# Kernel optimization log

Measured on AMD Instinct MI355X. Metric: run time of the kernel, lower is better.

Reference implementation:

```python
import jax, jax.numpy as jnp
import numpy as np

B, S, D, H = 8, 1024, 1024, 16
DEPTH = D // H  # 64


def setup_inputs() -> dict:
    key = jax.random.key(0)
    ks = jax.random.split(key, 12)
    s = 1.0 / np.sqrt(D)
    return {
        "Q": jax.random.normal(ks[0], (B, S, D), jnp.float32),
        "K": jax.random.normal(ks[1], (B, S, D), jnp.float32),
        "V": jax.random.normal(ks[2], (B, S, D), jnp.float32),
        "mask": jnp.zeros((B, 1, 1, S), jnp.float32),
        "Wq": jax.random.normal(ks[3], (D, D), jnp.float32) * s,
        "bq": jnp.zeros((D,), jnp.float32),
        "Wk": jax.random.normal(ks[4], (D, D), jnp.float32) * s,
        "bk": jnp.zeros((D,), jnp.float32),
        "Wv": jax.random.normal(ks[5], (D, D), jnp.float32) * s,
        "bv": jnp.zeros((D,), jnp.float32),
        "Wo": jax.random.normal(ks[6], (D, D), jnp.float32) * s,
        "bo": jnp.zeros((D,), jnp.float32),
    }


def _split_heads(x):
    # [B,S,D] -> [B,H,S,depth]
    b, s, _ = x.shape
    return x.reshape(b, s, H, DEPTH).transpose(0, 2, 1, 3)


def reference(Q, K, V, mask, Wq, bq, Wk, bk, Wv, bv, Wo, bo):
    q = _split_heads(Q @ Wq + bq)  # [B,H,S,depth]
    k = _split_heads(K @ Wk + bk)
    v = _split_heads(V @ Wv + bv)
    scale = 1.0 / jnp.sqrt(jnp.asarray(DEPTH, q.dtype))
    scores = jnp.einsum('bhqd,bhkd->bhqk', q, k) * scale  # [B,H,Sq,Sk]
    scores = scores + mask * (-1e9)
    attn = jax.nn.softmax(scores, axis=-1)
    out = jnp.einsum('bhqk,bhkd->bhqd', attn, v)  # [B,H,S,depth]
    out = out.transpose(0, 2, 1, 3).reshape(Q.shape[0], Q.shape[1], D)
    out = out @ Wo + bo
    return out, attn
```

## Files before the change

### kernel.cpp

```cpp
#include <hip/hip_runtime.h>

#define Bb 8
#define Ss 1024
#define Dd 1024
#define Hh 16
#define DEPTHh 64
#define BSD (Bb*Ss*Dd)
#define DDn (Dd*Dd)

typedef __bf16 bf16x8 __attribute__((ext_vector_type(8)));
typedef float  f32x4  __attribute__((ext_vector_type(4)));

__device__ __forceinline__ unsigned short f2bf(float f){
  unsigned u = __float_as_uint(f);
  u = (u + 0x7fffu + ((u >> 16) & 1u)) >> 16;
  return (unsigned short)u;
}
__device__ __forceinline__ float bf2f(unsigned short h){
  return __uint_as_float(((unsigned)h) << 16);
}

__global__ __launch_bounds__(256) void cvt_bf16(const float4* __restrict__ in,
                                                ushort4* __restrict__ out, int n4){
  int i = blockIdx.x*256 + threadIdx.x;
  if (i >= n4) return;
  float4 v = in[i];
  ushort4 o; o.x = f2bf(v.x); o.y = f2bf(v.y); o.z = f2bf(v.z); o.w = f2bf(v.w);
  out[i] = o;
}

__global__ __launch_bounds__(256) void transpose_w(const float* __restrict__ W,
                                                   ushort* __restrict__ WT){
  __shared__ float tl[32][33];
  int tx = threadIdx.x, ty = threadIdx.y;
  int bx = blockIdx.x*32, by = blockIdx.y*32;
  #pragma unroll
  for (int i=0;i<32;i+=8) tl[ty+i][tx] = W[(by+ty+i)*Dd + bx+tx];
  __syncthreads();
  #pragma unroll
  for (int i=0;i<32;i+=8) WT[(bx+ty+i)*Dd + by+tx] = f2bf(tl[tx][ty+i]);
}

__global__ __launch_bounds__(512) void transpose_v(const ushort* __restrict__ vh,
                                                   ushort* __restrict__ vt){
  __shared__ ushort tl[64][65];
  int tx = threadIdx.x, ty = threadIdx.y;
  long base = (long)blockIdx.y * 65536;
  int s0 = blockIdx.x*64;
  #pragma unroll
  for (int i=0;i<64;i+=8) tl[ty+i][tx] = vh[base + (long)(s0+ty+i)*64 + tx];
  __syncthreads();
  #pragma unroll
  for (int i=0;i<64;i+=8) vt[base + (long)(ty+i)*1024 + s0 + tx] = tl[tx][ty+i];
}

enum { M_PROJ=0, M_FINAL=3 };

template<int MODE>
__global__ __launch_bounds__(256) void gemm_bt(
    const ushort* __restrict__ Aall, const ushort* __restrict__ Ball,
    int lda, int ldb, int K, long sA, long sB,
    float* __restrict__ outf, ushort* __restrict__ outh,
    const float* __restrict__ aux)
{
  __shared__ ushort As[64][40];
  __shared__ ushort Bs[64][40];
  const int z = blockIdx.z;
  const ushort* A  = Aall + (long)z*sA;
  const ushort* Bp = Ball + (long)z*sB;
  const int m0 = blockIdx.x*64, n0 = blockIdx.y*64;
  const int t = threadIdx.x;
  const int lane = t & 63, wave = t >> 6;
  const int wm = (wave>>1)*32, wn = (wave&1)*32;
  const int q = lane>>4, l16 = lane&15;
  const int srow = t>>2, scol = (t&3)*8;

  f32x4 acc[2][2] = {};

  for (int k0=0; k0<K; k0+=32){
    uint4 av = *(const uint4*)(A  + (long)(m0+srow)*lda + k0 + scol);
    uint4 bv = *(const uint4*)(Bp + (long)(n0+srow)*ldb + k0 + scol);
    __syncthreads();
    *(uint4*)(&As[srow][scol]) = av;
    *(uint4*)(&Bs[srow][scol]) = bv;
    __syncthreads();
    bf16x8 a0 = *(const bf16x8*)(&As[wm      + l16][q*8]);
    bf16x8 a1 = *(const bf16x8*)(&As[wm + 16 + l16][q*8]);
    bf16x8 b0 = *(const bf16x8*)(&Bs[wn      + l16][q*8]);
    bf16x8 b1 = *(const bf16x8*)(&Bs[wn + 16 + l16][q*8]);
    acc[0][0] = __builtin_amdgcn_mfma_f32_16x16x32_bf16(a0,b0,acc[0][0],0,0,0);
    acc[0][1] = __builtin_amdgcn_mfma_f32_16x16x32_bf16(a0,b1,acc[0][1],0,0,0);
    acc[1][0] = __builtin_amdgcn_mfma_f32_16x16x32_bf16(a1,b0,acc[1][0],0,0,0);
    acc[1][1] = __builtin_amdgcn_mfma_f32_16x16x32_bf16(a1,b1,acc[1][1],0,0,0);
  }

  #pragma unroll
  for (int ti=0; ti<2; ti++)
  #pragma unroll
  for (int tj=0; tj<2; tj++)
  #pragma unroll
  for (int r=0; r<4; r++){
    float v = acc[ti][tj][r];
    const int row = m0 + wm + ti*16 + q*4 + r;
    const int col = n0 + wn + tj*16 + l16;
    if (MODE == M_PROJ){
      v += aux[col];
      const int b = row>>10, s = row&1023, h = col>>6, d = col&63;
      outh[((long)((b*Hh + h)*Ss + s)<<6) + d] = f2bf(v);
    } else {
      v += aux[col];
      outf[(long)row*Dd + col] = v;
    }
  }
}

__global__ __launch_bounds__(256) void attn_fused(
    const ushort* __restrict__ qh,
    const ushort* __restrict__ kh,
    const ushort* __restrict__ vt,
    const float*  __restrict__ mask,
    float* __restrict__ attn_f,
    ushort* __restrict__ concat)
{
  __shared__ __align__(16) ushort qs[64][72];
  __shared__ __align__(16) ushort ks[64][72];
  __shared__ __align__(16) ushort vs[64][72];
  __shared__ __align__(16) ushort ps[64][72];
  __shared__ float red_m[2][64];
  __shared__ float red_l[2][64];

  const int z = blockIdx.z;
  const int b = z >> 4, h = z & 15;
  const int t = threadIdx.x;
  const int lane = t & 63, wave = t >> 6;
  const int wm = (wave >> 1) * 32;
  const int wc = wave & 1;
  const int wn = wc * 32;
  const int q = lane >> 4, l16 = lane & 15;
  const int srow = t >> 2, sc = (t & 3) * 8;

  const ushort* qz = qh + ((long)z << 16);
  const ushort* kz = kh + ((long)z << 16);
  const ushort* vz = vt + ((long)z << 16);
  const int q0 = blockIdx.x * 64;

  {
    const ushort* src = qz + (long)(q0 + srow) * 64 + sc;
    *(uint4*)(&qs[srow][sc])      = *(const uint4*)(src);
    *(uint4*)(&qs[srow][sc + 32]) = *(const uint4*)(src + 32);
  }

  float m_ln[2][4], l_ln[2][4];
  #pragma unroll
  for (int ti=0; ti<2; ti++)
  #pragma unroll
  for (int r=0; r<4; r++){ m_ln[ti][r] = -1e30f; l_ln[ti][r] = 0.f; }

  for (int s = 0; s < 16; ++s){
    const int k0 = s * 64;
    const ushort* ksrc = kz + (long)(k0 + srow) * 64 + sc;
    uint4 kv0 = *(const uint4*)(ksrc);
    uint4 kv1 = *(const uint4*)(ksrc + 32);
    __syncthreads();
    *(uint4*)(&ks[srow][sc])      = kv0;
    *(uint4*)(&ks[srow][sc + 32]) = kv1;
    __syncthreads();

    f32x4 accs[2][2] = {};
    #pragma unroll
    for (int kk=0; kk<2; ++kk){
      bf16x8 a0 = *(const bf16x8*)(&qs[wm      + l16][kk*32 + q*8]);
      bf16x8 a1 = *(const bf16x8*)(&qs[wm + 16 + l16][kk*32 + q*8]);
      bf16x8 b0 = *(const bf16x8*)(&ks[wn      + l16][kk*32 + q*8]);
      bf16x8 b1 = *(const bf16x8*)(&ks[wn + 16 + l16][kk*32 + q*8]);
      accs[0][0] = __builtin_amdgcn_mfma_f32_16x16x32_bf16(a0,b0,accs[0][0],0,0,0);
      accs[0][1] = __builtin_amdgcn_mfma_f32_16x16x32_bf16(a0,b1,accs[0][1],0,0,0);
      accs[1][0] = __builtin_amdgcn_mfma_f32_16x16x32_bf16(a1,b0,accs[1][0],0,0,0);
      accs[1][1] = __builtin_amdgcn_mfma_f32_16x16x32_bf16(a1,b1,accs[1][1],0,0,0);
    }
    const float mk0 = mask[(b<<10) + k0 + wn + l16]      * (-1e9f);
    const float mk1 = mask[(b<<10) + k0 + wn + 16 + l16] * (-1e9f);
    #pragma unroll
    for (int ti=0; ti<2; ti++)
    #pragma unroll
    for (int r=0; r<4; r++){
      const float s0 = accs[ti][0][r]*0.125f + mk0;
      const float s1 = accs[ti][1][r]*0.125f + mk1;
      const float mn = fmaxf(m_ln[ti][r], fmaxf(s0, s1));
      l_ln[ti][r] = l_ln[ti][r]*__expf(m_ln[ti][r]-mn)
                  + __expf(s0-mn) + __expf(s1-mn);
      m_ln[ti][r] = mn;
    }
  }

  #pragma unroll
  for (int ti=0; ti<2; ti++)
  #pragma unroll
  for (int r=0; r<4; r++){
    float m = m_ln[ti][r], l = l_ln[ti][r];
    #pragma unroll
    for (int off=1; off<16; off<<=1){
      float om = __shfl_xor(m, off, 64);
      float ol = __shfl_xor(l, off, 64);
      float mn = fmaxf(m, om);
      l = l*__expf(m-mn) + ol*__expf(om-mn);
      m = mn;
    }
    m_ln[ti][r] = m; l_ln[ti][r] = l;
  }
  if (l16 == 0){
    #pragma unroll
    for (int ti=0; ti<2; ti++)
    #pragma unroll
    for (int r=0; r<4; r++){
      const int row = wm + ti*16 + q*4 + r;
      red_m[wc][row] = m_ln[ti][r];
      red_l[wc][row] = l_ln[ti][r];
    }
  }
  __syncthreads();
  float m_fin[2][4], li[2][4];
  #pragma unroll
  for (int ti=0; ti<2; ti++)
  #pragma unroll
  for (int r=0; r<4; r++){
    const int row = wm + ti*16 + q*4 + r;
    const float m0 = red_m[0][row], m1 = red_m[1][row];
    const float l0 = red_l[0][row], l1 = red_l[1][row];
    const float mt = fmaxf(m0, m1);
    const float lt = l0*__expf(m0-mt) + l1*__expf(m1-mt);
    m_fin[ti][r] = mt;
    li[ti][r] = 1.0f / lt;
  }

  f32x4 accp[2][2] = {};
  for (int s = 0; s < 16; ++s){
    const int k0 = s * 64;
    const ushort* ksrc = kz + (long)(k0 + srow) * 64 + sc;
    const ushort* vsrc = vz + (long)srow * 1024 + k0 + sc;
    uint4 kv0 = *(const uint4*)(ksrc);
    uint4 kv1 = *(const uint4*)(ksrc + 32);
    uint4 vv0 = *(const uint4*)(vsrc);
    uint4 vv1 = *(const uint4*)(vsrc + 32);
    __syncthreads();
    *(uint4*)(&ks[srow][sc])      = kv0;
    *(uint4*)(&ks[srow][sc + 32]) = kv1;
    *(uint4*)(&vs[srow][sc])      = vv0;
    *(uint4*)(&vs[srow][sc + 32]) = vv1;
    __syncthreads();

    f32x4 accs[2][2] = {};
    #pragma unroll
    for (int kk=0; kk<2; ++kk){
      bf16x8 a0 = *(const bf16x8*)(&qs[wm      + l16][kk*32 + q*8]);
      bf16x8 a1 = *(const bf16x8*)(&qs[wm + 16 + l16][kk*32 + q*8]);
      bf16x8 b0 = *(const bf16x8*)(&ks[wn      + l16][kk*32 + q*8]);
      bf16x8 b1 = *(const bf16x8*)(&ks[wn + 16 + l16][kk*32 + q*8]);
      accs[0][0] = __builtin_amdgcn_mfma_f32_16x16x32_bf16(a0,b0,accs[0][0],0,0,0);
      accs[0][1] = __builtin_amdgcn_mfma_f32_16x16x32_bf16(a0,b1,accs[0][1],0,0,0);
      accs[1][0] = __builtin_amdgcn_mfma_f32_16x16x32_bf16(a1,b0,accs[1][0],0,0,0);
      accs[1][1] = __builtin_amdgcn_mfma_f32_16x16x32_bf16(a1,b1,accs[1][1],0,0,0);
    }
    const float mk0 = mask[(b<<10) + k0 + wn + l16]      * (-1e9f);
    const float mk1 = mask[(b<<10) + k0 + wn + 16 + l16] * (-1e9f);
    #pragma unroll
    for (int ti=0; ti<2; ti++)
    #pragma unroll
    for (int r=0; r<4; r++){
      const int row = wm + ti*16 + q*4 + r;
      const float p0 = __expf(accs[ti][0][r]*0.125f + mk0 - m_fin[ti][r]) * li[ti][r];
      const float p1 = __expf(accs[ti][1][r]*0.125f + mk1 - m_fin[ti][r]) * li[ti][r];
      float* arow = attn_f + (((long)z<<20) + ((long)(q0+row)<<10) + k0);
      arow[wn + l16]      = p0;
      arow[wn + 16 + l16] = p1;
      ps[row][wn + l16]      = f2bf(p0);
      ps[row][wn + 16 + l16] = f2bf(p1);
    }
    __syncthreads();
    #pragma unroll
    for (int kk=0; kk<2; ++kk){
      bf16x8 a0 = *(const bf16x8*)(&ps[wm      + l16][kk*32 + q*8]);
      bf16x8 a1 = *(const bf16x8*)(&ps[wm + 16 + l16][kk*32 + q*8]);
      bf16x8 b0 = *(const bf16x8*)(&vs[wn      + l16][kk*32 + q*8]);
      bf16x8 b1 = *(const bf16x8*)(&vs[wn + 16 + l16][kk*32 + q*8]);
      accp[0][0] = __builtin_amdgcn_mfma_f32_16x16x32_bf16(a0,b0,accp[0][0],0,0,0);
      accp[0][1] = __builtin_amdgcn_mfma_f32_16x16x32_bf16(a0,b1,accp[0][1],0,0,0);
      accp[1][0] = __builtin_amdgcn_mfma_f32_16x16x32_bf16(a1,b0,accp[1][0],0,0,0);
      accp[1][1] = __builtin_amdgcn_mfma_f32_16x16x32_bf16(a1,b1,accp[1][1],0,0,0);
    }
  }

  #pragma unroll
  for (int mi=0; mi<2; mi++)
  #pragma unroll
  for (int nj=0; nj<2; nj++)
  #pragma unroll
  for (int r=0; r<4; r++){
    const int row = q0 + wm + mi*16 + q*4 + r;
    const int d   = wn + nj*16 + l16;
    concat[(((long)(b<<10) + row)<<10) + (h<<6) + d] = f2bf(accp[mi][nj][r]);
  }
}

extern "C" void kernel_launch(void* const* d_in, const int* in_sizes, int n_in,
                              void* d_out, int out_size, void* d_ws, size_t ws_size,
                              hipStream_t stream)
{
  (void)in_sizes; (void)n_in; (void)out_size; (void)ws_size;
  const float* Q    = (const float*)d_in[0];
  const float* Kin  = (const float*)d_in[1];
  const float* V    = (const float*)d_in[2];
  const float* mask = (const float*)d_in[3];
  const float* Wq   = (const float*)d_in[4];
  const float* bq   = (const float*)d_in[5];
  const float* Wk   = (const float*)d_in[6];
  const float* bk   = (const float*)d_in[7];
  const float* Wv   = (const float*)d_in[8];
  const float* bv   = (const float*)d_in[9];
  const float* Wo   = (const float*)d_in[10];
  const float* bo   = (const float*)d_in[11];
  float* out    = (float*)d_out;
  float* attn_f = out + (long)BSD;

  ushort* ws     = (ushort*)d_ws;
  ushort* Xq     = ws;
  ushort* Xk     = Xq  + (long)BSD;
  ushort* Xv     = Xk  + (long)BSD;
  ushort* WqT    = Xv  + (long)BSD;
  ushort* WkT    = WqT + (long)DDn;
  ushort* WvT    = WkT + (long)DDn;
  ushort* WoT    = WvT + (long)DDn;
  ushort* qh     = WoT + (long)DDn;
  ushort* kh     = qh  + (long)BSD;
  ushort* vt     = kh  + (long)BSD;
  ushort* vh     = vt  + (long)BSD;
  ushort* concat = Xq;

  cvt_bf16<<<dim3(BSD/4/256), 256, 0, stream>>>((const float4*)Q,   (ushort4*)Xq, BSD/4);
  cvt_bf16<<<dim3(BSD/4/256), 256, 0, stream>>>((const float4*)Kin, (ushort4*)Xk, BSD/4);
  cvt_bf16<<<dim3(BSD/4/256), 256, 0, stream>>>((const float4*)V,   (ushort4*)Xv, BSD/4);

  transpose_w<<<dim3(32,32), dim3(32,8), 0, stream>>>(Wq, WqT);
  transpose_w<<<dim3(32,32), dim3(32,8), 0, stream>>>(Wk, WkT);
  transpose_w<<<dim3(32,32), dim3(32,8), 0, stream>>>(Wv, WvT);
  transpose_w<<<dim3(32,32), dim3(32,8), 0, stream>>>(Wo, WoT);

  gemm_bt<M_PROJ><<<dim3(128,16,1), 256, 0, stream>>>(Xq, WqT, Dd, Dd, Dd, 0,0, nullptr, qh, bq);
  gemm_bt<M_PROJ><<<dim3(128,16,1), 256, 0, stream>>>(Xk, WkT, Dd, Dd, Dd, 0,0, nullptr, kh, bk);
  gemm_bt<M_PROJ><<<dim3(128,16,1), 256, 0, stream>>>(Xv, WvT, Dd, Dd, Dd, 0,0, nullptr, vh, bv);

  transpose_v<<<dim3(16,128), dim3(64,8), 0, stream>>>(vh, vt);

  attn_fused<<<dim3(16,1,128), 256, 0, stream>>>(qh, kh, vt, mask, attn_f, concat);

  gemm_bt<M_FINAL><<<dim3(128,16,1), 256, 0, stream>>>(concat, WoT, Dd, Dd, Dd,
                                                       0,0, out, nullptr, bo);
}
```

Baseline: 955.7 us.

## Use 128x128 GEMM tiles with direct-to-LDS loads and prefetch K/V in attention

Replaces the 64x64 projection GEMM with a 128x128 tile kernel that copies A/B straight into LDS via global_load_lds and keeps a 4x4 MFMA accumulator grid per wave. This raises data reuse per loaded tile and skips the register staging step. The attention kernel now computes K·Q^T with keys as rows, so per-query softmax statistics live in lanes and fewer shuffles are needed. It also switches to exp2 with folded scaling, caches the mask in LDS, register-prefetches the next K/V tile, and writes attention probabilities as float4. The larger GEMM accumulator raises register pressure, and the GEMM loop has no double buffering.

```diff
diff --git a/kernel.cpp b/kernel.cpp
--- a/kernel.cpp
+++ b/kernel.cpp
@@ -4,7 +4,6 @@
 #define Ss 1024
 #define Dd 1024
 #define Hh 16
-#define DEPTHh 64
 #define BSD (Bb*Ss*Dd)
 #define DDn (Dd*Dd)
 
@@ -16,8 +15,12 @@
   u = (u + 0x7fffu + ((u >> 16) & 1u)) >> 16;
   return (unsigned short)u;
 }
-__device__ __forceinline__ float bf2f(unsigned short h){
-  return __uint_as_float(((unsigned)h) << 16);
+__device__ __forceinline__ float fexp2(float x){ return __builtin_exp2f(x); }
+
+__device__ __forceinline__ void gload16(const ushort* g, ushort* l){
+  __builtin_amdgcn_global_load_lds(
+      (const __attribute__((address_space(1))) void*)g,
+      (__attribute__((address_space(3))) void*)l, 16, 0, 0);
 }
 
 __global__ __launch_bounds__(256) void cvt_bf16(const float4* __restrict__ in,
@@ -57,58 +60,64 @@
 enum { M_PROJ=0, M_FINAL=3 };
 
 template<int MODE>
-__global__ __launch_bounds__(256) void gemm_bt(
-    const ushort* __restrict__ Aall, const ushort* __restrict__ Ball,
-    int lda, int ldb, int K, long sA, long sB,
+__global__ __launch_bounds__(256) void gemm128(
+    const ushort* __restrict__ A, const ushort* __restrict__ B,
     float* __restrict__ outf, ushort* __restrict__ outh,
     const float* __restrict__ aux)
 {
-  __shared__ ushort As[64][40];
-  __shared__ ushort Bs[64][40];
-  const int z = blockIdx.z;
-  const ushort* A  = Aall + (long)z*sA;
-  const ushort* Bp = Ball + (long)z*sB;
-  const int m0 = blockIdx.x*64, n0 = blockIdx.y*64;
-  const int t = threadIdx.x;
-  const int lane = t & 63, wave = t >> 6;
-  const int wm = (wave>>1)*32, wn = (wave&1)*32;
+  __shared__ __align__(16) ushort As[128*32];
+  __shared__ __align__(16) ushort Bs[128*32];
+  const int t = threadIdx.x, lane = t & 63, wave = t >> 6;
+  const int m0 = blockIdx.x*128, n0 = blockIdx.y*128;
+  const int wm = (wave>>1)*64, wn = (wave&1)*64;
   const int q = lane>>4, l16 = lane&15;
-  const int srow = t>>2, scol = (t&3)*8;
-
-  f32x4 acc[2][2] = {};
-
-  for (int k0=0; k0<K; k0+=32){
-    uint4 av = *(const uint4*)(A  + (long)(m0+srow)*lda + k0 + scol);
-    uint4 bv = *(const uint4*)(Bp + (long)(n0+srow)*ldb + k0 + scol);
-    __syncthreads();
-    *(uint4*)(&As[srow][scol]) = av;
-    *(uint4*)(&Bs[srow][scol]) = bv;
-    __syncthreads();
-    bf16x8 a0 = *(const bf16x8*)(&As[wm      + l16][q*8]);
-    bf16x8 a1 = *(const bf16x8*)(&As[wm + 16 + l16][q*8]);
-    bf16x8 b0 = *(const bf16x8*)(&Bs[wn      + l16][q*8]);
-    bf16x8 b1 = *(const bf16x8*)(&Bs[wn + 16 + l16][q*8]);
-    acc[0][0] = __builtin_amdgcn_mfma_f32_16x16x32_bf16(a0,b0,acc[0][0],0,0,0);
-    acc[0][1] = __builtin_amdgcn_mfma_f32_16x16x32_bf16(a0,b1,acc[0][1],0,0,0);
-    acc[1][0] = __builtin_amdgcn_mfma_f32_16x16x32_bf16(a1,b0,acc[1][0],0,0,0);
-    acc[1][1] = __builtin_amdgcn_mfma_f32_16x16x32_bf16(a1,b1,acc[1][1],0,0,0);
-  }
-
-  #pragma unroll
-  for (int ti=0; ti<2; ti++)
-  #pragma unroll
-  for (int tj=0; tj<2; tj++)
-  #pragma unroll
-  for (int r=0; r<4; r++){
-    float v = acc[ti][tj][r];
-    const int row = m0 + wm + ti*16 + q*4 + r;
-    const int col = n0 + wn + tj*16 + l16;
+  const int row0 = t>>2, cc = (t&3)*8;
+
+  ushort* lA0 = As + wave*512;
+  ushort* lA1 = As + 2048 + wave*512;
+  ushort* lB0 = Bs + wave*512;
+  ushort* lB1 = Bs + 2048 + wave*512;
+  const ushort* gA0 = A + (long)(m0+row0)*Dd + cc;
+  const ushort* gA1 = A + (long)(m0+row0+64)*Dd + cc;
+  const ushort* gB0 = B + (long)(n0+row0)*Dd + cc;
+  const ushort* gB1 = B + (long)(n0+row0+64)*Dd + cc;
+
+  f32x4 acc[4][4] = {};
+
+  for (int k0=0; k0<Dd; k0+=32){
+    __syncthreads();
+    gload16(gA0+k0, lA0);
+    gload16(gA1+k0, lA1);
+    gload16(gB0+k0, lB0);
+    gload16(gB1+k0, lB1);
+    __syncthreads();
+    bf16x8 af[4], bfr[4];
+    #pragma unroll
+    for (int i=0;i<4;i++){
+      af[i]  = *(const bf16x8*)(As + (wm+i*16+l16)*32 + q*8);
+      bfr[i] = *(const bf16x8*)(Bs + (wn+i*16+l16)*32 + q*8);
+    }
+    #pragma unroll
+    for (int mi=0;mi<4;mi++)
+    #pragma unroll
+    for (int nj=0;nj<4;nj++)
+      acc[mi][nj] = __builtin_amdgcn_mfma_f32_16x16x32_bf16(af[mi],bfr[nj],acc[mi][nj],0,0,0);
+  }
+
+  #pragma unroll
+  for (int mi=0;mi<4;mi++)
+  #pragma unroll
+  for (int nj=0;nj<4;nj++)
+  #pragma unroll
+  for (int r=0;r<4;r++){
+    float v = acc[mi][nj][r];
+    const int row = m0 + wm + mi*16 + q*4 + r;
+    const int col = n0 + wn + nj*16 + l16;
+    v += aux[col];
     if (MODE == M_PROJ){
-      v += aux[col];
       const int b = row>>10, s = row&1023, h = col>>6, d = col&63;
       outh[((long)((b*Hh + h)*Ss + s)<<6) + d] = f2bf(v);
     } else {
-      v += aux[col];
       outf[(long)row*Dd + col] = v;
     }
   }
@@ -126,6 +135,7 @@
   __shared__ __align__(16) ushort ks[64][72];
   __shared__ __align__(16) ushort vs[64][72];
   __shared__ __align__(16) ushort ps[64][72];
+  __shared__ float msk[64];
   __shared__ float red_m[2][64];
   __shared__ float red_l[2][64];
 
@@ -143,6 +153,9 @@
   const ushort* kz = kh + ((long)z << 16);
   const ushort* vz = vt + ((long)z << 16);
   const int q0 = blockIdx.x * 64;
+  const float LOG2E = 1.44269504f;
+  const float SC2   = 0.125f * LOG2E;
+  const float MSC2  = -1e9f * LOG2E;
 
   {
     const ushort* src = qz + (long)(q0 + srow) * 64 + sc;
@@ -150,131 +163,147 @@
     *(uint4*)(&qs[srow][sc + 32]) = *(const uint4*)(src + 32);
   }
 
-  float m_ln[2][4], l_ln[2][4];
-  #pragma unroll
-  for (int ti=0; ti<2; ti++)
-  #pragma unroll
-  for (int r=0; r<4; r++){ m_ln[ti][r] = -1e30f; l_ln[ti][r] = 0.f; }
-
+  float m2[2], lsum[2];
+  m2[0] = m2[1] = -1e30f; lsum[0] = lsum[1] = 0.f;
+
+  uint4 kv0, kv1; float mv;
+  {
+    const ushort* ksrc = kz + (long)srow * 64 + sc;
+    kv0 = *(const uint4*)(ksrc); kv1 = *(const uint4*)(ksrc + 32);
+    mv = (t < 64) ? mask[(b<<10) + t] * MSC2 : 0.f;
+  }
   for (int s = 0; s < 16; ++s){
-    const int k0 = s * 64;
-    const ushort* ksrc = kz + (long)(k0 + srow) * 64 + sc;
-    uint4 kv0 = *(const uint4*)(ksrc);
-    uint4 kv1 = *(const uint4*)(ksrc + 32);
     __syncthreads();
     *(uint4*)(&ks[srow][sc])      = kv0;
     *(uint4*)(&ks[srow][sc + 32]) = kv1;
-    __syncthreads();
+    if (t < 64) msk[t] = mv;
+    __syncthreads();
+    if (s < 15){
+      const ushort* ksrc = kz + (long)((s+1)*64 + srow) * 64 + sc;
+      kv0 = *(const uint4*)(ksrc); kv1 = *(const uint4*)(ksrc + 32);
+      if (t < 64) mv = mask[(b<<10) + (s+1)*64 + t] * MSC2;
+    }
 
     f32x4 accs[2][2] = {};
     #pragma unroll
     for (int kk=0; kk<2; ++kk){
-      bf16x8 a0 = *(const bf16x8*)(&qs[wm      + l16][kk*32 + q*8]);
-      bf16x8 a1 = *(const bf16x8*)(&qs[wm + 16 + l16][kk*32 + q*8]);
-      bf16x8 b0 = *(const bf16x8*)(&ks[wn      + l16][kk*32 + q*8]);
-      bf16x8 b1 = *(const bf16x8*)(&ks[wn + 16 + l16][kk*32 + q*8]);
+      bf16x8 a0 = *(const bf16x8*)(&ks[wm      + l16][kk*32 + q*8]);
+      bf16x8 a1 = *(const bf16x8*)(&ks[wm + 16 + l16][kk*32 + q*8]);
+      bf16x8 b0 = *(const bf16x8*)(&qs[wn      + l16][kk*32 + q*8]);
+      bf16x8 b1 = *(const bf16x8*)(&qs[wn + 16 + l16][kk*32 + q*8]);
       accs[0][0] = __builtin_amdgcn_mfma_f32_16x16x32_bf16(a0,b0,accs[0][0],0,0,0);
       accs[0][1] = __builtin_amdgcn_mfma_f32_16x16x32_bf16(a0,b1,accs[0][1],0,0,0);
       accs[1][0] = __builtin_amdgcn_mfma_f32_16x16x32_bf16(a1,b0,accs[1][0],0,0,0);
       accs[1][1] = __builtin_amdgcn_mfma_f32_16x16x32_bf16(a1,b1,accs[1][1],0,0,0);
     }
-    const float mk0 = mask[(b<<10) + k0 + wn + l16]      * (-1e9f);
-    const float mk1 = mask[(b<<10) + k0 + wn + 16 + l16] * (-1e9f);
-    #pragma unroll
-    for (int ti=0; ti<2; ti++)
-    #pragma unroll
-    for (int r=0; r<4; r++){
-      const float s0 = accs[ti][0][r]*0.125f + mk0;
-      const float s1 = accs[ti][1][r]*0.125f + mk1;
-      const float mn = fmaxf(m_ln[ti][r], fmaxf(s0, s1));
-      l_ln[ti][r] = l_ln[ti][r]*__expf(m_ln[ti][r]-mn)
-                  + __expf(s0-mn) + __expf(s1-mn);
-      m_ln[ti][r] = mn;
-    }
-  }
-
-  #pragma unroll
-  for (int ti=0; ti<2; ti++)
-  #pragma unroll
-  for (int r=0; r<4; r++){
-    float m = m_ln[ti][r], l = l_ln[ti][r];
-    #pragma unroll
-    for (int off=1; off<16; off<<=1){
+    #pragma unroll
+    for (int tj=0; tj<2; ++tj){
+      float sv[8];
+      #pragma unroll
+      for (int ti=0; ti<2; ++ti)
+      #pragma unroll
+      for (int r=0; r<4; ++r){
+        const int key = wm + ti*16 + q*4 + r;
+        sv[ti*4+r] = accs[ti][tj][r]*SC2 + msk[key];
+      }
+      float mx01 = fmaxf(sv[0],sv[1]), mx23 = fmaxf(sv[2],sv[3]);
+      float mx45 = fmaxf(sv[4],sv[5]), mx67 = fmaxf(sv[6],sv[7]);
+      float mx = fmaxf(fmaxf(fmaxf(mx01,mx23), fmaxf(mx45,mx67)), m2[tj]);
+      float e0 = fexp2(sv[0]-mx), e1 = fexp2(sv[1]-mx);
+      float e2 = fexp2(sv[2]-mx), e3 = fexp2(sv[3]-mx);
+      float e4 = fexp2(sv[4]-mx), e5 = fexp2(sv[5]-mx);
+      float e6 = fexp2(sv[6]-mx), e7 = fexp2(sv[7]-mx);
+      float add = ((e0+e1)+(e2+e3)) + ((e4+e5)+(e6+e7));
+      lsum[tj] = lsum[tj]*fexp2(m2[tj]-mx) + add;
+      m2[tj] = mx;
+    }
+  }
+
+  #pragma unroll
+  for (int tj=0; tj<2; ++tj){
+    float m = m2[tj], l = lsum[tj];
+    #pragma unroll
+    for (int off=16; off<=32; off<<=1){
       float om = __shfl_xor(m, off, 64);
       float ol = __shfl_xor(l, off, 64);
       float mn = fmaxf(m, om);
-      l = l*__expf(m-mn) + ol*__expf(om-mn);
+      l = l*fexp2(m-mn) + ol*fexp2(om-mn);
       m = mn;
     }
-    m_ln[ti][r] = m; l_ln[ti][r] = l;
-  }
-  if (l16 == 0){
-    #pragma unroll
-    for (int ti=0; ti<2; ti++)
-    #pragma unroll
-    for (int r=0; r<4; r++){
-      const int row = wm + ti*16 + q*4 + r;
-      red_m[wc][row] = m_ln[ti][r];
-      red_l[wc][row] = l_ln[ti][r];
+    m2[tj] = m; lsum[tj] = l;
+  }
+  if (lane < 16){
+    #pragma unroll
+    for (int tj=0; tj<2; ++tj){
+      red_m[wave>>1][wn + tj*16 + l16] = m2[tj];
+      red_l[wave>>1][wn + tj*16 + l16] = lsum[tj];
     }
   }
   __syncthreads();
-  float m_fin[2][4], li[2][4];
-  #pragma unroll
-  for (int ti=0; ti<2; ti++)
-  #pragma unroll
-  for (int r=0; r<4; r++){
-    const int row = wm + ti*16 + q*4 + r;
-    const float m0 = red_m[0][row], m1 = red_m[1][row];
-    const float l0 = red_l[0][row], l1 = red_l[1][row];
-    const float mt = fmaxf(m0, m1);
-    const float lt = l0*__expf(m0-mt) + l1*__expf(m1-mt);
-    m_fin[ti][r] = mt;
-    li[ti][r] = 1.0f / lt;
+  float m2f[2], li[2];
+  #pragma unroll
+  for (int tj=0; tj<2; ++tj){
+    const int query = wn + tj*16 + l16;
+    const float ma = red_m[0][query], mb = red_m[1][query];
+    const float la = red_l[0][query], lb = red_l[1][query];
+    const float mt = fmaxf(ma, mb);
+    m2f[tj] = mt;
+    li[tj]  = 1.0f / (la*fexp2(ma-mt) + lb*fexp2(mb-mt));
   }
 
   f32x4 accp[2][2] = {};
+  uint4 vv0, vv1;
+  {
+    const ushort* ksrc = kz + (long)srow * 64 + sc;
+    kv0 = *(const uint4*)(ksrc); kv1 = *(const uint4*)(ksrc + 32);
+    const ushort* vsrc = vz + (long)srow * 1024 + sc;
+    vv0 = *(const uint4*)(vsrc); vv1 = *(const uint4*)(vsrc + 32);
+    mv = (t < 64) ? mask[(b<<10) + t] * MSC2 : 0.f;
+  }
   for (int s = 0; s < 16; ++s){
     const int k0 = s * 64;
-    const ushort* ksrc = kz + (long)(k0 + srow) * 64 + sc;
-    const ushort* vsrc = vz + (long)srow * 1024 + k0 + sc;
-    uint4 kv0 = *(const uint4*)(ksrc);
-    uint4 kv1 = *(const uint4*)(ksrc + 32);
-    uint4 vv0 = *(const uint4*)(vsrc);
-    uint4 vv1 = *(const uint4*)(vsrc + 32);
     __syncthreads();
     *(uint4*)(&ks[srow][sc])      = kv0;
     *(uint4*)(&ks[srow][sc + 32]) = kv1;
     *(uint4*)(&vs[srow][sc])      = vv0;
     *(uint4*)(&vs[srow][sc + 32]) = vv1;
-    __syncthreads();
+    if (t < 64) msk[t] = mv;
+    __syncthreads();
+    if (s < 15){
+      const ushort* ksrc = kz + (long)(k0 + 64 + srow) * 64 + sc;
+      kv0 = *(const uint4*)(ksrc); kv1 = *(const uint4*)(ksrc + 32);
+      const ushort* vsrc = vz + (long)srow * 1024 + k0 + 64 + sc;
+      vv0 = *(const uint4*)(vsrc); vv1 = *(const uint4*)(vsrc + 32);
+      if (t < 64) mv = mask[(b<<10) + k0 + 64 + t] * MSC2;
+    }
 
     f32x4 accs[2][2] = {};
     #pragma unroll
     for (int kk=0; kk<2; ++kk){
-      bf16x8 a0 = *(const bf16x8*)(&qs[wm      + l16][kk*32 + q*8]);
-      bf16x8 a1 = *(const bf16x8*)(&qs[wm + 16 + l16][kk*32 + q*8]);
-      bf16x8 b0 = *(const bf16x8*)(&ks[wn      + l16][kk*32 + q*8]);
-      bf16x8 b1 = *(const bf16x8*)(&ks[wn + 16 + l16][kk*32 + q*8]);
+      bf16x8 a0 = *(const bf16x8*)(&ks[wm      + l16][kk*32 + q*8]);
+      bf16x8 a1 = *(const bf16x8*)(&ks[wm + 16 + l16][kk*32 + q*8]);
+      bf16x8 b0 = *(const bf16x8*)(&qs[wn      + l16][kk*32 + q*8]);
+      bf16x8 b1 = *(const bf16x8*)(&qs[wn + 16 + l16][kk*32 + q*8]);
       accs[0][0] = __builtin_amdgcn_mfma_f32_16x16x32_bf16(a0,b0,accs[0][0],0,0,0);
       accs[0][1] = __builtin_amdgcn_mfma_f32_16x16x32_bf16(a0,b1,accs[0][1],0,0,0);
       accs[1][0] = __builtin_amdgcn_mfma_f32_16x16x32_bf16(a1,b0,accs[1][0],0,0,0);
       accs[1][1] = __builtin_amdgcn_mfma_f32_16x16x32_bf16(a1,b1,accs[1][1],0,0,0);
     }
-    const float mk0 = mask[(b<<10) + k0 + wn + l16]      * (-1e9f);
-    const float mk1 = mask[(b<<10) + k0 + wn + 16 + l16] * (-1e9f);
-    #pragma unroll
-    for (int ti=0; ti<2; ti++)
-    #pragma unroll
-    for (int r=0; r<4; r++){
-      const int row = wm + ti*16 + q*4 + r;
-      const float p0 = __expf(accs[ti][0][r]*0.125f + mk0 - m_fin[ti][r]) * li[ti][r];
-      const float p1 = __expf(accs[ti][1][r]*0.125f + mk1 - m_fin[ti][r]) * li[ti][r];
-      float* arow = attn_f + (((long)z<<20) + ((long)(q0+row)<<10) + k0);
-      arow[wn + l16]      = p0;
-      arow[wn + 16 + l16] = p1;
-      ps[row][wn + l16]      = f2bf(p0);
-      ps[row][wn + 16 + l16] = f2bf(p1);
+    #pragma unroll
+    for (int ti=0; ti<2; ++ti)
+    #pragma unroll
+    for (int tj=0; tj<2; ++tj){
+      const int keyb  = wm + ti*16 + q*4;
+      const int query = wn + tj*16 + l16;
+      float4 pv;
+      pv.x = fexp2(accs[ti][tj][0]*SC2 + msk[keyb+0] - m2f[tj]) * li[tj];
+      pv.y = fexp2(accs[ti][tj][1]*SC2 + msk[keyb+1] - m2f[tj]) * li[tj];
+      pv.z = fexp2(accs[ti][tj][2]*SC2 + msk[keyb+2] - m2f[tj]) * li[tj];
+      pv.w = fexp2(accs[ti][tj][3]*SC2 + msk[keyb+3] - m2f[tj]) * li[tj];
+      *(float4*)(attn_f + ((long)z<<20) + ((long)(q0+query)<<10) + k0 + keyb) = pv;
+      ushort4 pb;
+      pb.x = f2bf(pv.x); pb.y = f2bf(pv.y); pb.z = f2bf(pv.z); pb.w = f2bf(pv.w);
+      *(ushort4*)(&ps[query][keyb]) = pb;
     }
     __syncthreads();
     #pragma unroll
@@ -345,14 +374,13 @@
   transpose_w<<<dim3(32,32), dim3(32,8), 0, stream>>>(Wv, WvT);
   transpose_w<<<dim3(32,32), dim3(32,8), 0, stream>>>(Wo, WoT);
 
-  gemm_bt<M_PROJ><<<dim3(128,16,1), 256, 0, stream>>>(Xq, WqT, Dd, Dd, Dd, 0,0, nullptr, qh, bq);
-  gemm_bt<M_PROJ><<<dim3(128,16,1), 256, 0, stream>>>(Xk, WkT, Dd, Dd, Dd, 0,0, nullptr, kh, bk);
-  gemm_bt<M_PROJ><<<dim3(128,16,1), 256, 0, stream>>>(Xv, WvT, Dd, Dd, Dd, 0,0, nullptr, vh, bv);
+  gemm128<M_PROJ><<<dim3(64,8,1), 256, 0, stream>>>(Xq, WqT, nullptr, qh, bq);
+  gemm128<M_PROJ><<<dim3(64,8,1), 256, 0, stream>>>(Xk, WkT, nullptr, kh, bk);
+  gemm128<M_PROJ><<<dim3(64,8,1), 256, 0, stream>>>(Xv, WvT, nullptr, vh, bv);
 
   transpose_v<<<dim3(16,128), dim3(64,8), 0, stream>>>(vh, vt);
 
   attn_fused<<<dim3(16,1,128), 256, 0, stream>>>(qh, kh, vt, mask, attn_f, concat);
 
-  gemm_bt<M_FINAL><<<dim3(128,16,1), 256, 0, stream>>>(concat, WoT, Dd, Dd, Dd,
-                                                       0,0, out, nullptr, bo);
-}
+  gemm128<M_FINAL><<<dim3(64,8,1), 256, 0, stream>>>(concat, WoT, out, nullptr, bo);
+}
```

Result: faster. 916.9 us (-4.1%).
